# Optimization experiments

Measured on AMD Instinct MI355X. Metric: run time of the kernel, lower is better.

## Reference

```python
import jax, jax.numpy as jnp
import numpy as np

B, T, I, H, O = 8192, 128, 28, 200, 10


def setup_inputs() -> dict:
    key = jax.random.key(0)
    ks = jax.random.split(key, 7)
    s_ih = 1.0 / np.sqrt(H)
    return {
        "x": jax.random.normal(ks[0], (B, T, I), dtype=jnp.float32),
        "W_ih": jax.random.uniform(ks[1], (H, I), jnp.float32, -s_ih, s_ih),
        "W_hh": jax.random.uniform(ks[2], (H, H), jnp.float32, -s_ih, s_ih),
        "b_ih": jax.random.uniform(ks[3], (H,), jnp.float32, -s_ih, s_ih),
        "b_hh": jax.random.uniform(ks[4], (H,), jnp.float32, -s_ih, s_ih),
        "W_fc": jax.random.uniform(ks[5], (O, H), jnp.float32, -s_ih, s_ih),
        "b_fc": jax.random.uniform(ks[6], (O,), jnp.float32, -s_ih, s_ih),
    }


def reference(x, W_ih, W_hh, b_ih, b_hh, W_fc, b_fc):
    # Precompute input projections for all timesteps in one GEMM: [B,T,H]
    xp = jnp.einsum("bti,hi->bth", x, W_ih) + b_ih + b_hh
    h0 = jnp.zeros((x.shape[0], W_hh.shape[0]), dtype=x.dtype)

    def step(h, xp_t):
        # h_t = relu(x_t W_ih^T + b_ih + h_{t-1} W_hh^T + b_hh)
        h = jax.nn.relu(xp_t + h @ W_hh.T)
        return h, None

    # scan over time: xp transposed to [T,B,H]
    h_last, _ = jax.lax.scan(step, h0, jnp.swapaxes(xp, 0, 1))
    # out[:, -1, :] then fc1
    return h_last @ W_fc.T + b_fc
```

## Files before the change

kernel.cpp:

```cpp
#include <hip/hip_runtime.h>

typedef float f4v __attribute__((ext_vector_type(4)));
typedef short s8v __attribute__((ext_vector_type(8)));

#define TT 128
#define II 28
#define HH 200
#define BB 16
#define NT 512
#define CH 8
#define KX 224
#define NCH (TT / CH)

template <bool B> struct BC { static constexpr bool value = B; };

__device__ __forceinline__ unsigned pk_hu(float a, float b) {
    unsigned ua = __builtin_bit_cast(unsigned, a) + 0x8000u;
    unsigned ub = __builtin_bit_cast(unsigned, b) + 0x8000u;
    return __builtin_amdgcn_perm(ub, ua, 0x07060302);
}
__device__ __forceinline__ short f2bf(float f) {
    return (short)((__builtin_bit_cast(unsigned, f) + 0x8000u) >> 16);
}
__device__ __forceinline__ float bf2f(short s) {
    return __builtin_bit_cast(float, ((unsigned)(unsigned short)s) << 16);
}

#define STEP_BAR() asm volatile("s_waitcnt lgkmcnt(0)\n\ts_barrier" ::: "memory")
#define VSTEP_BAR() asm volatile("s_waitcnt vmcnt(0) lgkmcnt(0)\n\ts_barrier" ::: "memory")

__global__ __launch_bounds__(NT, 4)
void rnn_r11(const float* __restrict__ x,
             const float* __restrict__ W_ih,
             const float* __restrict__ W_hh,
             const float* __restrict__ b_ih,
             const float* __restrict__ b_hh,
             const float* __restrict__ W_fc,
             const float* __restrict__ b_fc,
             float* __restrict__ out)
{
    __shared__ __align__(16) short Hf[2][7][512];
    __shared__ __align__(16) short Xf[2][CH][512];
    __shared__ __align__(16) float Xl[CH * BB * II];

    const int tid  = threadIdx.x;
    const int lane = tid & 63;
    const int q    = lane >> 4;
    const int lr   = lane & 15;
    const int wave = __builtin_amdgcn_readfirstlane(tid >> 6);
    const int b0   = blockIdx.x * BB;

    const bool two = (wave < 5);
    const int jt0  = two ? 2 * wave : 10 + (wave - 5);
    const int jt1  = two ? 2 * wave + 1 : 13;

    const int nIss = (wave < 6) ? 2 : 1;
    const int e0   = (wave < 6) ? 2 * wave : 12 + (wave - 6);
    unsigned xoff[2];
    #pragma unroll
    for (int k = 0; k < 2; ++k) {
        const int e  = e0 + k;
        const int m  = (e << 6) + lane;
        const int tl = m / 112;
        const int rm = m - tl * 112;
        const int r  = rm / 7;
        const int c4 = rm - r * 7;
        xoff[k] = (unsigned)(((((b0 + r) * TT + tl) * II) + c4 * 4) * 4);
    }
    auto issue_dma = [&](int c) {
        #pragma unroll
        for (int k = 0; k < 2; ++k) {
            if (k < nIss) {
                const char* src = (const char*)x + (xoff[k] + (unsigned)c * (CH * II * 4));
                float* dst = &Xl[(e0 + k) * 256];
                __builtin_amdgcn_global_load_lds(
                    (const __attribute__((address_space(1))) void*)src,
                    (__attribute__((address_space(3))) void*)dst, 16, 0, 0);
            }
        }
    };

    auto prepass = [&](int tc) {
        if (tid < 448) {
            const f4v v0 = *(const f4v*)&Xl[tid * 8];
            const f4v v1 = *(const f4v*)&Xl[tid * 8 + 4];
            const unsigned d[4] = { pk_hu(v0.x, v0.y), pk_hu(v0.z, v0.w),
                                    pk_hu(v1.x, v1.y), pk_hu(v1.z, v1.w) };
            int* dstb = ((int*)Xf) + (tc & 1) * 2048;
            #pragma unroll
            for (int dk = 0; dk < 4; ++dk) {
                const int kk = tid * 4 + dk;
                const int t  = kk / 224;
                const int k2 = kk - t * 224;
                const int r  = k2 / 14;
                const int cp = k2 - r * 14;
                dstb[t * 256 + 64 * (cp >> 2) + 4 * r + (cp & 3)] = (int)d[dk];
            }
        }
    };

    issue_dma(0);

    s8v Af[2][8];
    #pragma unroll
    for (int u = 0; u < 2; ++u) {
        const int j = 16 * (u ? jt1 : jt0) + lr;
        #pragma unroll
        for (int kc = 0; kc < 8; ++kc) {
            union { short s[8]; s8v v; } tv;
            #pragma unroll
            for (int i = 0; i < 8; ++i) {
                const int k = 32 * kc + 8 * q + i;
                float w = 0.0f;
                if (j < HH) {
                    if (k < HH)                     w = W_hh[j * HH + k];
                    else if (k >= KX && k < KX+II)  w = W_ih[j * II + (k - KX)];
                    else if (k == KX + II) {
                        w = b_ih[j] + b_hh[j];
                    } else if (k == KX + II + 1) {
                        const float bs = b_ih[j] + b_hh[j];
                        w = bs - bf2f(f2bf(bs));
                    }
                }
                tv.s[i] = f2bf(w);
            }
            Af[u][kc] = tv.v;
        }
    }

    for (int i = tid; i < 2 * 7 * 512 / 2; i += NT) ((int*)Hf)[i] = 0;
    for (int i = tid; i < 2 * CH * 512 / 2; i += NT)
        ((int*)Xf)[i] = (((i & 255) >= 194) && ((i & 3) == 2)) ? 0x3f803f80 : 0;

    const int j0w = 16 * jt0 + 4 * q;
    short* st0 = &Hf[0][j0w >> 5][(16 * ((j0w >> 3) & 3) + lr) * 8 + (j0w & 7)];
    const int j1w = 16 * jt1 + 4 * q;
    short* st1 = &Hf[0][j1w >> 5][(16 * ((j1w >> 3) & 3) + lr) * 8 + (j1w & 7)];
    const int HFH = 7 * 512;

    __syncthreads();
    prepass(0);
    STEP_BAR();
    issue_dma(1);

    const f4v Z = {0.f, 0.f, 0.f, 0.f};

    auto chunk = [&](int c, auto TWOC) {
        constexpr bool TWO = decltype(TWOC)::value;
        const short* xbase = &Xf[c & 1][0][0];
        #pragma unroll
        for (int s = 0; s < CH; ++s) {
            const int pb = s & 1;
            const short* hf = &Hf[pb][0][lane * 8];
            const s8v xb = *(const s8v*)&xbase[s * 512 + lane * 8];
            f4v a0, a1;
            if constexpr (TWO) {
                s8v g0 = *(const s8v*)(hf);
                s8v g1 = *(const s8v*)(hf + 512);
                s8v g2 = *(const s8v*)(hf + 1024);
                s8v g3 = *(const s8v*)(hf + 1536);
                a0 = __builtin_amdgcn_mfma_f32_16x16x32_bf16(Af[0][7], xb, Z, 0, 0, 0);
                a1 = __builtin_amdgcn_mfma_f32_16x16x32_bf16(Af[1][7], xb, Z, 0, 0, 0);
                a0 = __builtin_amdgcn_mfma_f32_16x16x32_bf16(Af[0][0], g0, a0, 0, 0, 0);
                a1 = __builtin_amdgcn_mfma_f32_16x16x32_bf16(Af[1][0], g0, a1, 0, 0, 0);
                g0 = *(const s8v*)(hf + 2048);
                a0 = __builtin_amdgcn_mfma_f32_16x16x32_bf16(Af[0][1], g1, a0, 0, 0, 0);
                a1 = __builtin_amdgcn_mfma_f32_16x16x32_bf16(Af[1][1], g1, a1, 0, 0, 0);
                g1 = *(const s8v*)(hf + 2560);
                a0 = __builtin_amdgcn_mfma_f32_16x16x32_bf16(Af[0][2], g2, a0, 0, 0, 0);
                a1 = __builtin_amdgcn_mfma_f32_16x16x32_bf16(Af[1][2], g2, a1, 0, 0, 0);
                g2 = *(const s8v*)(hf + 3072);
                a0 = __builtin_amdgcn_mfma_f32_16x16x32_bf16(Af[0][3], g3, a0, 0, 0, 0);
                a1 = __builtin_amdgcn_mfma_f32_16x16x32_bf16(Af[1][3], g3, a1, 0, 0, 0);
                a0 = __builtin_amdgcn_mfma_f32_16x16x32_bf16(Af[0][4], g0, a0, 0, 0, 0);
                a1 = __builtin_amdgcn_mfma_f32_16x16x32_bf16(Af[1][4], g0, a1, 0, 0, 0);
                a0 = __builtin_amdgcn_mfma_f32_16x16x32_bf16(Af[0][5], g1, a0, 0, 0, 0);
                a1 = __builtin_amdgcn_mfma_f32_16x16x32_bf16(Af[1][5], g1, a1, 0, 0, 0);
                a0 = __builtin_amdgcn_mfma_f32_16x16x32_bf16(Af[0][6], g2, a0, 0, 0, 0);
                a1 = __builtin_amdgcn_mfma_f32_16x16x32_bf16(Af[1][6], g2, a1, 0, 0, 0);
            } else {
                s8v g0 = *(const s8v*)(hf);
                s8v g1 = *(const s8v*)(hf + 1536);
                s8v g2 = *(const s8v*)(hf + 2048);
                s8v g3 = *(const s8v*)(hf + 2560);
                a0 = __builtin_amdgcn_mfma_f32_16x16x32_bf16(Af[0][7], xb, Z, 0, 0, 0);
                a1 = __builtin_amdgcn_mfma_f32_16x16x32_bf16(Af[0][3], g1, Z, 0, 0, 0);
                g1 = *(const s8v*)(hf + 512);
                a0 = __builtin_amdgcn_mfma_f32_16x16x32_bf16(Af[0][0], g0, a0, 0, 0, 0);
                g0 = *(const s8v*)(hf + 1024);
                a1 = __builtin_amdgcn_mfma_f32_16x16x32_bf16(Af[0][4], g2, a1, 0, 0, 0);
                g2 = *(const s8v*)(hf + 3072);
                a0 = __builtin_amdgcn_mfma_f32_16x16x32_bf16(Af[0][1], g1, a0, 0, 0, 0);
                a1 = __builtin_amdgcn_mfma_f32_16x16x32_bf16(Af[0][5], g3, a1, 0, 0, 0);
                a0 = __builtin_amdgcn_mfma_f32_16x16x32_bf16(Af[0][2], g0, a0, 0, 0, 0);
                a1 = __builtin_amdgcn_mfma_f32_16x16x32_bf16(Af[0][6], g2, a1, 0, 0, 0);
                a0 += a1;
            }
            {
                const int wo = (pb ^ 1) * HFH;
                int2 hv;
                hv.x = (int)pk_hu(fmaxf(a0.x, 0.f), fmaxf(a0.y, 0.f));
                hv.y = (int)pk_hu(fmaxf(a0.z, 0.f), fmaxf(a0.w, 0.f));
                *(int2*)(st0 + wo) = hv;
                if constexpr (TWO) {
                    hv.x = (int)pk_hu(fmaxf(a1.x, 0.f), fmaxf(a1.y, 0.f));
                    hv.y = (int)pk_hu(fmaxf(a1.z, 0.f), fmaxf(a1.w, 0.f));
                    *(int2*)(st1 + wo) = hv;
                }
            }
            if (s == 4 && c + 1 < NCH) prepass(c + 1);
            if (s == 5 && c + 2 < NCH) issue_dma(c + 2);
            if (s == 3) VSTEP_BAR();
            else        STEP_BAR();
        }
    };

    #pragma unroll 1
    for (int c = 0; c < NCH; ++c) {
        if (two) chunk(c, BC<true>{});
        else     chunk(c, BC<false>{});
    }

    __syncthreads();
    if (tid < BB * 10) {
        const int o = tid >> 4, r = tid & 15;
        const float* wrow = W_fc + o * HH;
        float acc = b_fc[o];
        #pragma unroll 1
        for (int kb = 0; kb < 25; ++kb) {
            const s8v hv = *(const s8v*)&Hf[0][kb >> 2][(16 * (kb & 3) + r) * 8];
            const f4v w0 = *(const f4v*)(wrow + kb * 8);
            const f4v w1 = *(const f4v*)(wrow + kb * 8 + 4);
            acc = fmaf(bf2f(hv[0]), w0.x, acc);
            acc = fmaf(bf2f(hv[1]), w0.y, acc);
            acc = fmaf(bf2f(hv[2]), w0.z, acc);
            acc = fmaf(bf2f(hv[3]), w0.w, acc);
            acc = fmaf(bf2f(hv[4]), w1.x, acc);
            acc = fmaf(bf2f(hv[5]), w1.y, acc);
            acc = fmaf(bf2f(hv[6]), w1.z, acc);
            acc = fmaf(bf2f(hv[7]), w1.w, acc);
        }
        __builtin_nontemporal_store(acc, &out[(long)(b0 + r) * 10 + o]);
    }
}

extern "C" void kernel_launch(void* const* d_in, const int* in_sizes, int n_in,
                              void* d_out, int out_size, void* d_ws, size_t ws_size,
                              hipStream_t stream) {
    const float* x    = (const float*)d_in[0];
    const float* W_ih = (const float*)d_in[1];
    const float* W_hh = (const float*)d_in[2];
    const float* b_ih = (const float*)d_in[3];
    const float* b_hh = (const float*)d_in[4];
    const float* W_fc = (const float*)d_in[5];
    const float* b_fc = (const float*)d_in[6];
    float* out = (float*)d_out;

    rnn_r11<<<dim3(8192 / BB), dim3(NT), 0, stream>>>(
        x, W_ih, W_hh, b_ih, b_hh, W_fc, b_fc, out);
}
```

Before: 278.6 us.

## Use 5 waves per block with up to three hidden tiles per wave

Shrinks the block from 8 to 5 waves, so each wave computes 3 (or 2) of the 13 hidden-dimension 16-row tiles instead of 2 (or 1 split across two accumulators). Fewer waves per block means each per-timestep barrier has fewer participants and more MFMA work sits between LDS reads of h, and the x DMA and bf16 prepass are redistributed to match. In exchange, per-wave register use grows (three weight-fragment sets and accumulators), the launch bound drops to 3 blocks per CU, and each wave's serial MFMA chain per step gets longer.

```diff
diff --git a/kernel.cpp b/kernel.cpp
--- a/kernel.cpp
+++ b/kernel.cpp
@@ -7,12 +7,12 @@
 #define II 28
 #define HH 200
 #define BB 16
-#define NT 512
+#define NT 320
 #define CH 8
 #define KX 224
 #define NCH (TT / CH)
 
-template <bool B> struct BC { static constexpr bool value = B; };
+template <int N> struct IC { static constexpr int value = N; };
 
 __device__ __forceinline__ unsigned pk_hu(float a, float b) {
     unsigned ua = __builtin_bit_cast(unsigned, a) + 0x8000u;
@@ -29,8 +29,8 @@
 #define STEP_BAR() asm volatile("s_waitcnt lgkmcnt(0)\n\ts_barrier" ::: "memory")
 #define VSTEP_BAR() asm volatile("s_waitcnt vmcnt(0) lgkmcnt(0)\n\ts_barrier" ::: "memory")
 
-__global__ __launch_bounds__(NT, 4)
-void rnn_r11(const float* __restrict__ x,
+__global__ __launch_bounds__(NT, 3)
+void rnn_r12(const float* __restrict__ x,
              const float* __restrict__ W_ih,
              const float* __restrict__ W_hh,
              const float* __restrict__ b_ih,
@@ -50,15 +50,14 @@
     const int wave = __builtin_amdgcn_readfirstlane(tid >> 6);
     const int b0   = blockIdx.x * BB;
 
-    const bool two = (wave < 5);
-    const int jt0  = two ? 2 * wave : 10 + (wave - 5);
-    const int jt1  = two ? 2 * wave + 1 : 13;
-
-    const int nIss = (wave < 6) ? 2 : 1;
-    const int e0   = (wave < 6) ? 2 * wave : 12 + (wave - 6);
-    unsigned xoff[2];
+    const int ntl  = (wave < 3) ? 3 : 2;
+    const int jtb  = (wave < 3) ? 3 * wave : 9 + 2 * (wave - 3);
+
+    const int nIss = (wave < 4) ? 3 : 2;
+    const int e0   = (wave < 4) ? 3 * wave : 12;
+    unsigned xoff[3];
     #pragma unroll
-    for (int k = 0; k < 2; ++k) {
+    for (int k = 0; k < 3; ++k) {
         const int e  = e0 + k;
         const int m  = (e << 6) + lane;
         const int tl = m / 112;
@@ -69,7 +68,7 @@
     }
     auto issue_dma = [&](int c) {
         #pragma unroll
-        for (int k = 0; k < 2; ++k) {
+        for (int k = 0; k < 3; ++k) {
             if (k < nIss) {
                 const char* src = (const char*)x + (xoff[k] + (unsigned)c * (CH * II * 4));
                 float* dst = &Xl[(e0 + k) * 256];
@@ -81,15 +80,19 @@
     };
 
     auto prepass = [&](int tc) {
-        if (tid < 448) {
-            const f4v v0 = *(const f4v*)&Xl[tid * 8];
-            const f4v v1 = *(const f4v*)&Xl[tid * 8 + 4];
-            const unsigned d[4] = { pk_hu(v0.x, v0.y), pk_hu(v0.z, v0.w),
-                                    pk_hu(v1.x, v1.y), pk_hu(v1.z, v1.w) };
+        if (tid < 224) {
+            const f4v v0 = *(const f4v*)&Xl[tid * 16];
+            const f4v v1 = *(const f4v*)&Xl[tid * 16 + 4];
+            const f4v v2 = *(const f4v*)&Xl[tid * 16 + 8];
+            const f4v v3 = *(const f4v*)&Xl[tid * 16 + 12];
+            const unsigned d[8] = { pk_hu(v0.x, v0.y), pk_hu(v0.z, v0.w),
+                                    pk_hu(v1.x, v1.y), pk_hu(v1.z, v1.w),
+                                    pk_hu(v2.x, v2.y), pk_hu(v2.z, v2.w),
+                                    pk_hu(v3.x, v3.y), pk_hu(v3.z, v3.w) };
             int* dstb = ((int*)Xf) + (tc & 1) * 2048;
             #pragma unroll
-            for (int dk = 0; dk < 4; ++dk) {
-                const int kk = tid * 4 + dk;
+            for (int dk = 0; dk < 8; ++dk) {
+                const int kk = tid * 8 + dk;
                 const int t  = kk / 224;
                 const int k2 = kk - t * 224;
                 const int r  = k2 / 14;
@@ -101,10 +104,10 @@
 
     issue_dma(0);
 
-    s8v Af[2][8];
+    s8v Af[3][8];
     #pragma unroll
-    for (int u = 0; u < 2; ++u) {
-        const int j = 16 * (u ? jt1 : jt0) + lr;
+    for (int u = 0; u < 3; ++u) {
+        const int j = 16 * (jtb + u) + lr;
         #pragma unroll
         for (int kc = 0; kc < 8; ++kc) {
             union { short s[8]; s8v v; } tv;
@@ -112,7 +115,7 @@
             for (int i = 0; i < 8; ++i) {
                 const int k = 32 * kc + 8 * q + i;
                 float w = 0.0f;
-                if (j < HH) {
+                if (u < ntl && j < HH) {
                     if (k < HH)                     w = W_hh[j * HH + k];
                     else if (k >= KX && k < KX+II)  w = W_ih[j * II + (k - KX)];
                     else if (k == KX + II) {
@@ -132,10 +135,12 @@
     for (int i = tid; i < 2 * CH * 512 / 2; i += NT)
         ((int*)Xf)[i] = (((i & 255) >= 194) && ((i & 3) == 2)) ? 0x3f803f80 : 0;
 
-    const int j0w = 16 * jt0 + 4 * q;
-    short* st0 = &Hf[0][j0w >> 5][(16 * ((j0w >> 3) & 3) + lr) * 8 + (j0w & 7)];
-    const int j1w = 16 * jt1 + 4 * q;
-    short* st1 = &Hf[0][j1w >> 5][(16 * ((j1w >> 3) & 3) + lr) * 8 + (j1w & 7)];
+    short* st[3];
+    #pragma unroll
+    for (int u = 0; u < 3; ++u) {
+        const int jw = 16 * (jtb + u) + 4 * q;
+        st[u] = &Hf[0][jw >> 5][(16 * ((jw >> 3) & 3) + lr) * 8 + (jw & 7)];
+    }
     const int HFH = 7 * 512;
 
     __syncthreads();
@@ -145,67 +150,61 @@
 
     const f4v Z = {0.f, 0.f, 0.f, 0.f};
 
-    auto chunk = [&](int c, auto TWOC) {
-        constexpr bool TWO = decltype(TWOC)::value;
+    auto chunk = [&](int c, auto NTC) {
+        constexpr int NTL = decltype(NTC)::value;
         const short* xbase = &Xf[c & 1][0][0];
         #pragma unroll
         for (int s = 0; s < CH; ++s) {
             const int pb = s & 1;
             const short* hf = &Hf[pb][0][lane * 8];
             const s8v xb = *(const s8v*)&xbase[s * 512 + lane * 8];
-            f4v a0, a1;
-            if constexpr (TWO) {
-                s8v g0 = *(const s8v*)(hf);
-                s8v g1 = *(const s8v*)(hf + 512);
-                s8v g2 = *(const s8v*)(hf + 1024);
-                s8v g3 = *(const s8v*)(hf + 1536);
-                a0 = __builtin_amdgcn_mfma_f32_16x16x32_bf16(Af[0][7], xb, Z, 0, 0, 0);
-                a1 = __builtin_amdgcn_mfma_f32_16x16x32_bf16(Af[1][7], xb, Z, 0, 0, 0);
-                a0 = __builtin_amdgcn_mfma_f32_16x16x32_bf16(Af[0][0], g0, a0, 0, 0, 0);
-                a1 = __builtin_amdgcn_mfma_f32_16x16x32_bf16(Af[1][0], g0, a1, 0, 0, 0);
-                g0 = *(const s8v*)(hf + 2048);
-                a0 = __builtin_amdgcn_mfma_f32_16x16x32_bf16(Af[0][1], g1, a0, 0, 0, 0);
-                a1 = __builtin_amdgcn_mfma_f32_16x16x32_bf16(Af[1][1], g1, a1, 0, 0, 0);
-                g1 = *(const s8v*)(hf + 2560);
-                a0 = __builtin_amdgcn_mfma_f32_16x16x32_bf16(Af[0][2], g2, a0, 0, 0, 0);
-                a1 = __builtin_amdgcn_mfma_f32_16x16x32_bf16(Af[1][2], g2, a1, 0, 0, 0);
-                g2 = *(const s8v*)(hf + 3072);
-                a0 = __builtin_amdgcn_mfma_f32_16x16x32_bf16(Af[0][3], g3, a0, 0, 0, 0);
-                a1 = __builtin_amdgcn_mfma_f32_16x16x32_bf16(Af[1][3], g3, a1, 0, 0, 0);
-                a0 = __builtin_amdgcn_mfma_f32_16x16x32_bf16(Af[0][4], g0, a0, 0, 0, 0);
-                a1 = __builtin_amdgcn_mfma_f32_16x16x32_bf16(Af[1][4], g0, a1, 0, 0, 0);
-                a0 = __builtin_amdgcn_mfma_f32_16x16x32_bf16(Af[0][5], g1, a0, 0, 0, 0);
-                a1 = __builtin_amdgcn_mfma_f32_16x16x32_bf16(Af[1][5], g1, a1, 0, 0, 0);
-                a0 = __builtin_amdgcn_mfma_f32_16x16x32_bf16(Af[0][6], g2, a0, 0, 0, 0);
-                a1 = __builtin_amdgcn_mfma_f32_16x16x32_bf16(Af[1][6], g2, a1, 0, 0, 0);
-            } else {
-                s8v g0 = *(const s8v*)(hf);
-                s8v g1 = *(const s8v*)(hf + 1536);
-                s8v g2 = *(const s8v*)(hf + 2048);
-                s8v g3 = *(const s8v*)(hf + 2560);
-                a0 = __builtin_amdgcn_mfma_f32_16x16x32_bf16(Af[0][7], xb, Z, 0, 0, 0);
-                a1 = __builtin_amdgcn_mfma_f32_16x16x32_bf16(Af[0][3], g1, Z, 0, 0, 0);
-                g1 = *(const s8v*)(hf + 512);
-                a0 = __builtin_amdgcn_mfma_f32_16x16x32_bf16(Af[0][0], g0, a0, 0, 0, 0);
-                g0 = *(const s8v*)(hf + 1024);
-                a1 = __builtin_amdgcn_mfma_f32_16x16x32_bf16(Af[0][4], g2, a1, 0, 0, 0);
-                g2 = *(const s8v*)(hf + 3072);
-                a0 = __builtin_amdgcn_mfma_f32_16x16x32_bf16(Af[0][1], g1, a0, 0, 0, 0);
-                a1 = __builtin_amdgcn_mfma_f32_16x16x32_bf16(Af[0][5], g3, a1, 0, 0, 0);
-                a0 = __builtin_amdgcn_mfma_f32_16x16x32_bf16(Af[0][2], g0, a0, 0, 0, 0);
-                a1 = __builtin_amdgcn_mfma_f32_16x16x32_bf16(Af[0][6], g2, a1, 0, 0, 0);
-                a0 += a1;
-            }
+            s8v g0 = *(const s8v*)(hf);
+            s8v g1 = *(const s8v*)(hf + 512);
+            s8v g2 = *(const s8v*)(hf + 1024);
+            s8v g3 = *(const s8v*)(hf + 1536);
+            f4v a0, a1, a2;
+            a0 = __builtin_amdgcn_mfma_f32_16x16x32_bf16(Af[0][7], xb, Z, 0, 0, 0);
+            if constexpr (NTL > 1) a1 = __builtin_amdgcn_mfma_f32_16x16x32_bf16(Af[1][7], xb, Z, 0, 0, 0);
+            if constexpr (NTL > 2) a2 = __builtin_amdgcn_mfma_f32_16x16x32_bf16(Af[2][7], xb, Z, 0, 0, 0);
+            a0 = __builtin_amdgcn_mfma_f32_16x16x32_bf16(Af[0][0], g0, a0, 0, 0, 0);
+            if constexpr (NTL > 1) a1 = __builtin_amdgcn_mfma_f32_16x16x32_bf16(Af[1][0], g0, a1, 0, 0, 0);
+            if constexpr (NTL > 2) a2 = __builtin_amdgcn_mfma_f32_16x16x32_bf16(Af[2][0], g0, a2, 0, 0, 0);
+            g0 = *(const s8v*)(hf + 2048);
+            a0 = __builtin_amdgcn_mfma_f32_16x16x32_bf16(Af[0][1], g1, a0, 0, 0, 0);
+            if constexpr (NTL > 1) a1 = __builtin_amdgcn_mfma_f32_16x16x32_bf16(Af[1][1], g1, a1, 0, 0, 0);
+            if constexpr (NTL > 2) a2 = __builtin_amdgcn_mfma_f32_16x16x32_bf16(Af[2][1], g1, a2, 0, 0, 0);
+            g1 = *(const s8v*)(hf + 2560);
+            a0 = __builtin_amdgcn_mfma_f32_16x16x32_bf16(Af[0][2], g2, a0, 0, 0, 0);
+            if constexpr (NTL > 1) a1 = __builtin_amdgcn_mfma_f32_16x16x32_bf16(Af[1][2], g2, a1, 0, 0, 0);
+            if constexpr (NTL > 2) a2 = __builtin_amdgcn_mfma_f32_16x16x32_bf16(Af[2][2], g2, a2, 0, 0, 0);
+            g2 = *(const s8v*)(hf + 3072);
+            a0 = __builtin_amdgcn_mfma_f32_16x16x32_bf16(Af[0][3], g3, a0, 0, 0, 0);
+            if constexpr (NTL > 1) a1 = __builtin_amdgcn_mfma_f32_16x16x32_bf16(Af[1][3], g3, a1, 0, 0, 0);
+            if constexpr (NTL > 2) a2 = __builtin_amdgcn_mfma_f32_16x16x32_bf16(Af[2][3], g3, a2, 0, 0, 0);
+            a0 = __builtin_amdgcn_mfma_f32_16x16x32_bf16(Af[0][4], g0, a0, 0, 0, 0);
+            if constexpr (NTL > 1) a1 = __builtin_amdgcn_mfma_f32_16x16x32_bf16(Af[1][4], g0, a1, 0, 0, 0);
+            if constexpr (NTL > 2) a2 = __builtin_amdgcn_mfma_f32_16x16x32_bf16(Af[2][4], g0, a2, 0, 0, 0);
+            a0 = __builtin_amdgcn_mfma_f32_16x16x32_bf16(Af[0][5], g1, a0, 0, 0, 0);
+            if constexpr (NTL > 1) a1 = __builtin_amdgcn_mfma_f32_16x16x32_bf16(Af[1][5], g1, a1, 0, 0, 0);
+            if constexpr (NTL > 2) a2 = __builtin_amdgcn_mfma_f32_16x16x32_bf16(Af[2][5], g1, a2, 0, 0, 0);
+            a0 = __builtin_amdgcn_mfma_f32_16x16x32_bf16(Af[0][6], g2, a0, 0, 0, 0);
+            if constexpr (NTL > 1) a1 = __builtin_amdgcn_mfma_f32_16x16x32_bf16(Af[1][6], g2, a1, 0, 0, 0);
+            if constexpr (NTL > 2) a2 = __builtin_amdgcn_mfma_f32_16x16x32_bf16(Af[2][6], g2, a2, 0, 0, 0);
             {
                 const int wo = (pb ^ 1) * HFH;
                 int2 hv;
                 hv.x = (int)pk_hu(fmaxf(a0.x, 0.f), fmaxf(a0.y, 0.f));
                 hv.y = (int)pk_hu(fmaxf(a0.z, 0.f), fmaxf(a0.w, 0.f));
-                *(int2*)(st0 + wo) = hv;
-                if constexpr (TWO) {
+                *(int2*)(st[0] + wo) = hv;
+                if constexpr (NTL > 1) {
                     hv.x = (int)pk_hu(fmaxf(a1.x, 0.f), fmaxf(a1.y, 0.f));
                     hv.y = (int)pk_hu(fmaxf(a1.z, 0.f), fmaxf(a1.w, 0.f));
-                    *(int2*)(st1 + wo) = hv;
+                    *(int2*)(st[1] + wo) = hv;
+                }
+                if constexpr (NTL > 2) {
+                    hv.x = (int)pk_hu(fmaxf(a2.x, 0.f), fmaxf(a2.y, 0.f));
+                    hv.y = (int)pk_hu(fmaxf(a2.z, 0.f), fmaxf(a2.w, 0.f));
+                    *(int2*)(st[2] + wo) = hv;
                 }
             }
             if (s == 4 && c + 1 < NCH) prepass(c + 1);
@@ -217,8 +216,8 @@
 
     #pragma unroll 1
     for (int c = 0; c < NCH; ++c) {
-        if (two) chunk(c, BC<true>{});
-        else     chunk(c, BC<false>{});
+        if (ntl == 3) chunk(c, IC<3>{});
+        else          chunk(c, IC<2>{});
     }
 
     __syncthreads();
@@ -256,6 +255,6 @@
     const float* b_fc = (const float*)d_in[6];
     float* out = (float*)d_out;
 
-    rnn_r11<<<dim3(8192 / BB), dim3(NT), 0, stream>>>(
+    rnn_r12<<<dim3(8192 / BB), dim3(NT), 0, stream>>>(
         x, W_ih, W_hh, b_ih, b_hh, W_fc, b_fc, out);
 }
```

Result: slower. 378.6 us (+35.9%).
